# Kernel tuning notes

Measured on AMD Instinct MI355X. Metric: run time of the kernel, lower is better.

The kernel has to match this reference:

```python
import jax, jax.numpy as jnp
import numpy as np

RX, RY = 10, 10  # box filter half-widths (Angle == 0 path)


def setup_inputs() -> dict:
    key = jax.random.key(0)
    x = jax.random.normal(key, (8, 1, 2048, 2048), dtype=jnp.float32)
    # Angle == 0: constant all-ones box kernel (1,1,2rx+1,2ry+1), a fixed buffer
    kernelx = jnp.ones((1, 1, 2 * RX + 1, 2 * RY + 1), dtype=jnp.float32)
    return {"x": x, "kernelx": kernelx}


def reference(x, kernelx):
    # circular pad: H by rx (top/bottom), W by ry (left/right), matching
    # F.pad(input, (ry, ry, rx, rx), mode='circular')
    xp = jnp.pad(x, ((0, 0), (0, 0), (RX, RX), (RY, RY)), mode="wrap")
    # valid conv with the box kernel -> output has the original HxW
    out = jax.lax.conv_general_dilated(
        xp, kernelx,
        window_strides=(1, 1),
        padding="VALID",
        dimension_numbers=("NCHW", "OIHW", "NCHW"),
    )
    return out
```

## Files before the change

kernel.cpp:

```cpp
#include <hip/hip_runtime.h>


#define HH 2048
#define WW 2048
#define RAD 10
#define DIAM 21
#define TH 32
#define TW 128
#define NQ 38
#define RROWS (TH + 20)
#define RQ (RROWS * NQ)
#define SSTR 156

typedef float nfloat4 __attribute__((ext_vector_type(4)));
typedef const __attribute__((address_space(1))) void* gp_t;
typedef __attribute__((address_space(3))) void* lp_t;

__global__ __launch_bounds__(256) void box_filter_v7(
    const float* __restrict__ x, float* __restrict__ out) {
  __shared__ float sRAW[RQ * 4];
  __shared__ float sCS[TH * SSTR];

  const int n = blockIdx.z;
  const int h0 = blockIdx.y * TH;
  const int w0 = blockIdx.x * TW;
  const float* __restrict__ xp = x + (size_t)n * (HH * WW);
  float* __restrict__ op = out + (size_t)n * (HH * WW);
  const int tid = threadIdx.x;

  {
    const int wbase = tid & ~63;
#pragma unroll
    for (int it = 0; it < 8; ++it) {
      const int idx = it * 256 + tid;
      if (idx < RQ) {
        const int r = idx / NQ;
        const int c = idx - r * NQ;
        const int grow = (h0 - RAD + r) & (HH - 1);
        const int gcol = (w0 - 12 + 4 * c) & (WW - 1);
        const float* src = xp + (size_t)grow * WW + gcol;
        float* dst = &sRAW[(size_t)(it * 256 + wbase) * 4];
        __builtin_amdgcn_global_load_lds((gp_t)(uintptr_t)src,
                                         (lp_t)(uintptr_t)dst, 16, 0, 0);
      }
    }
  }
  __syncthreads();

  if (tid < NQ * 2) {
    const int c4 = tid % NQ;
    const int g = tid / NQ;
    const float* base = &sRAW[((16 * g) * NQ + c4) * 4];
    nfloat4 s = *(const nfloat4*)base;
#pragma unroll
    for (int k = 1; k < DIAM; ++k)
      s += *(const nfloat4*)(base + k * (NQ * 4));
    *(nfloat4*)&sCS[(16 * g) * SSTR + 4 * c4] = s;
#pragma unroll
    for (int i = 1; i < 16; ++i) {
      s += *(const nfloat4*)(base + (i + 20) * (NQ * 4)) -
           *(const nfloat4*)(base + (i - 1) * (NQ * 4));
      *(nfloat4*)&sCS[(16 * g + i) * SSTR + 4 * c4] = s;
    }
  }
  __syncthreads();

  {
    const int r = tid >> 3;
    const int cg = tid & 7;
    const float* row = &sCS[r * SSTR + 16 * cg];
    float* orow = &op[(size_t)(h0 + r) * WW + w0 + 16 * cg];
    __align__(16) float w[40];
#pragma unroll
    for (int k = 0; k < 10; ++k)
      *(nfloat4*)&w[4 * k] = *(const nfloat4*)&row[4 * k];
    float s = w[2];
#pragma unroll
    for (int k = 3; k <= 22; ++k) s += w[k];
    float o[16];
    o[0] = s;
#pragma unroll
    for (int j = 1; j < 16; ++j) {
      s += w[j + 22] - w[j + 1];
      o[j] = s;
    }
#pragma unroll
    for (int q = 0; q < 4; ++q) {
      nfloat4 ov = {o[4 * q], o[4 * q + 1], o[4 * q + 2], o[4 * q + 3]};
      *(nfloat4*)&orow[4 * q] = ov;
    }
  }
}

extern "C" void kernel_launch(void* const* d_in, const int* in_sizes, int n_in,
                              void* d_out, int out_size, void* d_ws, size_t ws_size,
                              hipStream_t stream) {
  const float* x = (const float*)d_in[0];
  float* out = (float*)d_out;
  dim3 grid(WW / TW, HH / TH, 8);
  dim3 block(256);
  hipLaunchKernelGGL(box_filter_v7, grid, block, 0, stream, x, out);
}
```

Before: 239.5 us.

## Stream tall row panels through an LDS ring buffer to cut halo reloads

Each block now walks a 256-row panel in steps of 32 rows instead of handling one 32-row tile. A 64-row circular LDS buffer keeps the 20 halo rows from one step so they are reused by the next. This reduces the redundant global reads of vertical halo rows. In exchange the grid has 8x fewer blocks, and each step runs load, sync and compute in sequence. The vertical and horizontal passes also use only part of the threads, so latency hiding may suffer.

```diff
diff --git a/kernel.cpp b/kernel.cpp
--- a/kernel.cpp
+++ b/kernel.cpp
@@ -5,89 +5,106 @@
 #define WW 2048
 #define RAD 10
 #define DIAM 21
-#define TH 32
 #define TW 128
 #define NQ 38
-#define RROWS (TH + 20)
-#define RQ (RROWS * NQ)
+#define RING 64
+#define RW (NQ * 4)
+#define NT 8
+#define PANEL (32 * NT)
 #define SSTR 156
 
 typedef float nfloat4 __attribute__((ext_vector_type(4)));
 typedef const __attribute__((address_space(1))) void* gp_t;
 typedef __attribute__((address_space(3))) void* lp_t;
 
-__global__ __launch_bounds__(256) void box_filter_v7(
+#define STAGE(S0, NR)                                                         \
+  do {                                                                        \
+    const int slotbase = (S0) & 63;                                           \
+    _Pragma("unroll")                                                         \
+    for (int rd = 0; rd < ((NR) * NQ + 255) / 256; ++rd) {                    \
+      const int q = rd * 256 + tid;                                           \
+      if (q < (NR) * NQ) {                                                    \
+        const int rr = q / NQ;                                                \
+        const int c = q - rr * NQ;                                            \
+        const int grow = (hbase + (S0) + rr - 10) & (HH - 1);                 \
+        const int gcol = (w0 - 12 + 4 * c) & (WW - 1);                        \
+        const float* src = xp + (size_t)grow * WW + gcol;                     \
+        float* dst = (float*)&ring[slotbase * RW + (rd * 256 + wbase) * 4];   \
+        __builtin_amdgcn_global_load_lds((gp_t)(uintptr_t)src,                \
+                                         (lp_t)(uintptr_t)dst, 16, 0, 0);     \
+      }                                                                       \
+    }                                                                         \
+  } while (0)
+
+__global__ __launch_bounds__(256) void box_filter_v8(
     const float* __restrict__ x, float* __restrict__ out) {
-  __shared__ float sRAW[RQ * 4];
-  __shared__ float sCS[TH * SSTR];
+  __shared__ float ring[RING * RW];
+  __shared__ float sCS[16 * SSTR];
 
   const int n = blockIdx.z;
-  const int h0 = blockIdx.y * TH;
+  const int hbase = blockIdx.y * PANEL;
   const int w0 = blockIdx.x * TW;
   const float* __restrict__ xp = x + (size_t)n * (HH * WW);
   float* __restrict__ op = out + (size_t)n * (HH * WW);
   const int tid = threadIdx.x;
+  const int wbase = tid & ~63;
 
-  {
-    const int wbase = tid & ~63;
+  STAGE(0, 20);
+
+  for (int t = 0; t < NT; ++t) {
+    const int tbase = 32 * t;
+    STAGE(32 * t + 20, 12);
+    STAGE(32 * t + 32, 20);
+    __syncthreads();
+
 #pragma unroll
-    for (int it = 0; it < 8; ++it) {
-      const int idx = it * 256 + tid;
-      if (idx < RQ) {
-        const int r = idx / NQ;
-        const int c = idx - r * NQ;
-        const int grow = (h0 - RAD + r) & (HH - 1);
-        const int gcol = (w0 - 12 + 4 * c) & (WW - 1);
-        const float* src = xp + (size_t)grow * WW + gcol;
-        float* dst = &sRAW[(size_t)(it * 256 + wbase) * 4];
-        __builtin_amdgcn_global_load_lds((gp_t)(uintptr_t)src,
-                                         (lp_t)(uintptr_t)dst, 16, 0, 0);
+    for (int g = 0; g < 2; ++g) {
+      if (tid < 2 * NQ) {
+        const int c4 = tid % NQ;
+        const int sg = tid / NQ;
+        const int p0 = tbase + 16 * g + 8 * sg;
+        const int cof = c4 * 4;
+        nfloat4 s = *(const nfloat4*)&ring[(p0 & 63) * RW + cof];
+#pragma unroll
+        for (int k = 1; k < DIAM; ++k)
+          s += *(const nfloat4*)&ring[((p0 + k) & 63) * RW + cof];
+        *(nfloat4*)&sCS[(8 * sg) * SSTR + cof] = s;
+#pragma unroll
+        for (int i = 1; i < 8; ++i) {
+          s += *(const nfloat4*)&ring[((p0 + i + 20) & 63) * RW + cof] -
+               *(const nfloat4*)&ring[((p0 + i - 1) & 63) * RW + cof];
+          *(nfloat4*)&sCS[(8 * sg + i) * SSTR + cof] = s;
+        }
       }
-    }
-  }
-  __syncthreads();
+      __syncthreads();
 
-  if (tid < NQ * 2) {
-    const int c4 = tid % NQ;
-    const int g = tid / NQ;
-    const float* base = &sRAW[((16 * g) * NQ + c4) * 4];
-    nfloat4 s = *(const nfloat4*)base;
+      if (tid < 128) {
+        const int r = tid >> 3;
+        const int cg = tid & 7;
+        const int p = tbase + 16 * g + r;
+        const float* rowp = &sCS[r * SSTR + 16 * cg];
+        float* orow = &op[(size_t)(hbase + p) * WW + w0 + 16 * cg];
+        __align__(16) float w[40];
 #pragma unroll
-    for (int k = 1; k < DIAM; ++k)
-      s += *(const nfloat4*)(base + k * (NQ * 4));
-    *(nfloat4*)&sCS[(16 * g) * SSTR + 4 * c4] = s;
+        for (int k = 0; k < 10; ++k)
+          *(nfloat4*)&w[4 * k] = *(const nfloat4*)&rowp[4 * k];
+        float s = w[2];
 #pragma unroll
-    for (int i = 1; i < 16; ++i) {
-      s += *(const nfloat4*)(base + (i + 20) * (NQ * 4)) -
-           *(const nfloat4*)(base + (i - 1) * (NQ * 4));
-      *(nfloat4*)&sCS[(16 * g + i) * SSTR + 4 * c4] = s;
-    }
-  }
-  __syncthreads();
-
-  {
-    const int r = tid >> 3;
-    const int cg = tid & 7;
-    const float* row = &sCS[r * SSTR + 16 * cg];
-    float* orow = &op[(size_t)(h0 + r) * WW + w0 + 16 * cg];
-    __align__(16) float w[40];
+        for (int k = 3; k <= 22; ++k) s += w[k];
+        float o[16];
+        o[0] = s;
 #pragma unroll
-    for (int k = 0; k < 10; ++k)
-      *(nfloat4*)&w[4 * k] = *(const nfloat4*)&row[4 * k];
-    float s = w[2];
+        for (int j = 1; j < 16; ++j) {
+          s += w[j + 22] - w[j + 1];
+          o[j] = s;
+        }
 #pragma unroll
-    for (int k = 3; k <= 22; ++k) s += w[k];
-    float o[16];
-    o[0] = s;
-#pragma unroll
-    for (int j = 1; j < 16; ++j) {
-      s += w[j + 22] - w[j + 1];
-      o[j] = s;
-    }
-#pragma unroll
-    for (int q = 0; q < 4; ++q) {
-      nfloat4 ov = {o[4 * q], o[4 * q + 1], o[4 * q + 2], o[4 * q + 3]};
-      *(nfloat4*)&orow[4 * q] = ov;
+        for (int q = 0; q < 4; ++q) {
+          nfloat4 ov = {o[4 * q], o[4 * q + 1], o[4 * q + 2], o[4 * q + 3]};
+          *(nfloat4*)&orow[4 * q] = ov;
+        }
+      }
+      if (g == 0) __syncthreads();
     }
   }
 }
@@ -97,7 +114,7 @@
                               hipStream_t stream) {
   const float* x = (const float*)d_in[0];
   float* out = (float*)d_out;
-  dim3 grid(WW / TW, HH / TH, 8);
+  dim3 grid(WW / TW, HH / PANEL, 8);
   dim3 block(256);
-  hipLaunchKernelGGL(box_filter_v7, grid, block, 0, stream, x, out);
+  hipLaunchKernelGGL(box_filter_v8, grid, block, 0, stream, x, out);
 }
```

New measurement: 267.7 us. +11.8%, slower.
